# Performance work log

Measured on AMD Instinct MI355X. Metric: run time of the kernel, lower is better.

## Reference

```python
import jax, jax.numpy as jnp
import numpy as np

UNITS = 1024
B, T = 32, 2048


def setup_inputs() -> dict:
    key = jax.random.key(0)
    ks = jax.random.split(key, 8)
    s = 1.0 / np.sqrt(UNITS)
    return {
        "x": jax.random.normal(ks[0], (B, T, UNITS), dtype=jnp.float32),
        "hidden": jax.random.normal(ks[1], (B, UNITS), dtype=jnp.float32),
        "W1_w": jax.random.uniform(ks[2], (UNITS, UNITS), jnp.float32, -s, s),
        "W1_b": jax.random.uniform(ks[3], (UNITS,), jnp.float32, -s, s),
        "W2_w": jax.random.uniform(ks[4], (UNITS, UNITS), jnp.float32, -s, s),
        "W2_b": jax.random.uniform(ks[5], (UNITS,), jnp.float32, -s, s),
        "V_w": jax.random.uniform(ks[6], (1, UNITS), jnp.float32, -s, s),
        "V_b": jax.random.uniform(ks[7], (1,), jnp.float32, -s, s),
    }


def reference(x, hidden, W1_w, W1_b, W2_w, W2_b, V_w, V_b):
    # hidden.squeeze().unsqueeze(1): [B, U] -> [B, 1, U]
    h = hidden[:, None, :]
    # tanh(W1(x) + W2(hidden)): [B, T, U]
    att = jnp.tanh(
        jnp.einsum("btu,vu->btv", x, W1_w) + W1_b
        + jnp.einsum("bsu,vu->bsv", h, W2_w) + W2_b
    )
    # score = V(att): [B, T, 1]
    score = jnp.einsum("btu,ou->bto", att, V_w) + V_b
    # softmax over T, then squeeze().unsqueeze(1): [B, T, 1] -> [B, 1, T]
    attention_weights = jnp.swapaxes(jax.nn.softmax(score, axis=1), 1, 2)
    # bmm([B,1,T], [B,T,U]) -> [B,1,U]; squeeze().unsqueeze(0) -> [1, B, U]
    context_vector = jnp.matmul(attention_weights, x)[:, 0, :][None, :, :]
    return context_vector, attention_weights
```

## Files before the change

kernel.cpp:

```cpp
#include <hip/hip_runtime.h>
#include <hip/hip_bf16.h>
#include <cstdint>
#include <cstddef>

#define UNITS 1024
#define BDIM 32
#define TDIM 2048
#define M_TOT (BDIM*TDIM)
#define KDIM UNITS
#define NDIM UNITS
#define NPART 4

#define K2LOG2E 2.885390081777927f

typedef __attribute__((ext_vector_type(8))) short bf16x8;
typedef __attribute__((ext_vector_type(8))) unsigned short ushort8;
typedef __attribute__((ext_vector_type(4))) float f32x4;

__device__ __forceinline__ unsigned short f2bf(float f) {
  unsigned u = __float_as_uint(f);
  u += 0x7fffu + ((u >> 16) & 1u);
  return (unsigned short)(u >> 16);
}
__device__ __forceinline__ float bf2f(unsigned short h) {
  return __uint_as_float(((unsigned)h) << 16);
}

__global__ __launch_bounds__(256) void cvt_kernel(const float* __restrict__ src,
                                                  ushort* __restrict__ dst, int n8) {
  int i = blockIdx.x * blockDim.x + threadIdx.x;
  int stride = gridDim.x * blockDim.x;
  const float4* s4 = (const float4*)src;
  ushort8* d8 = (ushort8*)dst;
  for (; i < n8; i += stride) {
    float4 a = s4[2*i], b = s4[2*i+1];
    ushort8 o;
    o[0] = f2bf(a.x); o[1] = f2bf(a.y); o[2] = f2bf(a.z); o[3] = f2bf(a.w);
    o[4] = f2bf(b.x); o[5] = f2bf(b.y); o[6] = f2bf(b.z); o[7] = f2bf(b.w);
    d8[i] = o;
  }
}

__global__ __launch_bounds__(64) void prep_c_kernel(const float* __restrict__ W2w,
                                                    const float* __restrict__ hidden,
                                                    const float* __restrict__ W1b,
                                                    const float* __restrict__ W2b,
                                                    float* __restrict__ c) {
  int v = blockIdx.x;
  int l = threadIdx.x;
  float acc[BDIM];
  #pragma unroll
  for (int b = 0; b < BDIM; b++) acc[b] = 0.f;
  for (int u0 = 0; u0 < UNITS; u0 += 64) {
    float w = W2w[v*UNITS + u0 + l];
    #pragma unroll
    for (int b = 0; b < BDIM; b++) acc[b] += w * hidden[b*UNITS + u0 + l];
  }
  float bias = W1b[v] + W2b[v];
  #pragma unroll
  for (int b = 0; b < BDIM; b++) {
    float s = acc[b];
    #pragma unroll
    for (int off = 32; off > 0; off >>= 1) s += __shfl_xor(s, off);
    if (l == 0) c[b*UNITS + v] = s + bias;
  }
}

#define GLL(g, l) __builtin_amdgcn_global_load_lds(                              \
    (const __attribute__((address_space(1))) void*)(g),                          \
    (__attribute__((address_space(3))) void*)(l), 16, 0, 0)

__global__ __launch_bounds__(512, 2) void gemm_score_kernel(
    const ushort* __restrict__ A,
    const ushort* __restrict__ W,
    const float* __restrict__ c,
    const float* __restrict__ Vw,
    float* __restrict__ score)
{
  __shared__ ushort shb[65536];

  const int nt = blockIdx.x & 3;
  const int m0 = (blockIdx.x >> 2) * 256;
  const int n0 = nt * 256;
  const int bb = m0 >> 11;
  const int tid = threadIdx.x;
  const int wave = tid >> 6;
  const int l = tid & 63;
  const int lrow = l & 15;
  const int lq = l >> 4;
  const int wm = (wave >> 2) * 128;
  const int wn = (wave & 3) * 64;

  const int s_g = ((tid & 3) - (tid >> 3)) & 3;
  const ushort* sA = A + (size_t)(m0 + (tid >> 2)) * KDIM + s_g * 8;
  const ushort* sB = W + (size_t)(n0 + (tid >> 2)) * KDIM + s_g * 8;

  const int prot = (lq + (lrow >> 1)) & 3;
  const int a_off = (wm + lrow) * 32 + prot * 8;
  const int b_off = (wn + lrow) * 32 + prot * 8;

  f32x4 acc[8][4];
  #pragma unroll
  for (int i = 0; i < 8; i++)
    #pragma unroll
    for (int j = 0; j < 4; j++) acc[i][j] = (f32x4)0.f;

  #define STAGE_A(TAU, C) {                                                     \
    const ushort* g_ = sA + (TAU) * 64 + (C) * 32;                              \
    ushort* d_ = shb + ((2*(TAU)+(C)) & 3) * 8192 + wave * 512;                 \
    GLL(g_, d_);                                                                \
    GLL(g_ + (size_t)128 * KDIM, d_ + 4096); }
  #define STAGE_B(TAU, C) {                                                     \
    const ushort* g_ = sB + (TAU) * 64 + (C) * 32;                              \
    ushort* d_ = shb + 32768 + ((2*(TAU)+(C)) & 3) * 8192 + wave * 512;         \
    GLL(g_, d_);                                                                \
    GLL(g_ + (size_t)128 * KDIM, d_ + 4096); }

  bf16x8 bv[4];

  #define PHASE(TAU, C, IH, VM, DO_ST, ST_TAU, ST_C) {                          \
    const int aslot_ = ((2*(TAU)+(C)) & 3) * 8192;                              \
    const int bslot_ = 32768 + aslot_;                                          \
    bf16x8 av[4];                                                               \
    if ((IH) == 0) {                                                            \
      _Pragma("unroll")                                                         \
      for (int j = 0; j < 4; j++)                                               \
        bv[j] = *(const bf16x8*)(shb + bslot_ + b_off + j * 512);               \
    }                                                                           \
    _Pragma("unroll")                                                           \
    for (int i = 0; i < 4; i++)                                                 \
      av[i] = *(const bf16x8*)(shb + aslot_ + a_off + ((IH)*4 + i) * 512);      \
    if ((DO_ST) == 1) STAGE_A(ST_TAU, ST_C);                                    \
    if ((DO_ST) == 2) STAGE_B(ST_TAU, ST_C);                                    \
    __builtin_amdgcn_s_barrier();                                               \
    __builtin_amdgcn_s_setprio(1);                                              \
    _Pragma("unroll")                                                           \
    for (int i = 0; i < 4; i++)                                                 \
      _Pragma("unroll")                                                         \
      for (int j = 0; j < 4; j++)                                               \
        acc[(IH)*4 + i][j] =                                                    \
          __builtin_amdgcn_mfma_f32_16x16x32_bf16(av[i], bv[j],                 \
                                                  acc[(IH)*4 + i][j], 0, 0, 0); \
    __builtin_amdgcn_s_setprio(0);                                              \
    if ((VM) == 8) asm volatile("s_waitcnt vmcnt(8)" ::: "memory");             \
    if ((VM) == 4) asm volatile("s_waitcnt vmcnt(4)" ::: "memory");             \
    if ((VM) == 0) asm volatile("s_waitcnt vmcnt(0)" ::: "memory");             \
    __builtin_amdgcn_s_barrier();                                               \
    __builtin_amdgcn_sched_barrier(0);                                          \
  }

  STAGE_A(0, 0); STAGE_B(0, 0);
  STAGE_A(0, 1); STAGE_B(0, 1);
  STAGE_A(1, 0); STAGE_B(1, 0);
  asm volatile("s_waitcnt vmcnt(8)" ::: "memory");
  __builtin_amdgcn_s_barrier();
  __builtin_amdgcn_sched_barrier(0);

  #pragma unroll 1
  for (int tau = 0; tau < 14; ++tau) {
    PHASE(tau, 0, 0, -1, 1, tau + 1, 1);
    PHASE(tau, 0, 1,  8, 2, tau + 1, 1);
    PHASE(tau, 1, 0, -1, 1, tau + 2, 0);
    PHASE(tau, 1, 1,  8, 2, tau + 2, 0);
  }
  PHASE(14, 0, 0, -1, 1, 15, 1);
  PHASE(14, 0, 1,  8, 2, 15, 1);
  PHASE(14, 1, 0, -1, 0, 0, 0);
  PHASE(14, 1, 1,  4, 0, 0, 0);
  PHASE(15, 0, 0, -1, 0, 0, 0);
  PHASE(15, 0, 1,  0, 0, 0, 0);
  PHASE(15, 1, 0, -1, 0, 0, 0);
  PHASE(15, 1, 1, -1, 0, 0, 0);

  #undef PHASE
  #undef STAGE_A
  #undef STAGE_B

  float vw4[4], ck4[4];
  float vws = 0.f;
  #pragma unroll
  for (int j = 0; j < 4; j++) {
    int n = n0 + wn + j * 16 + lrow;
    float v = Vw[n];
    vw4[j] = v;
    vws += v;
    ck4[j] = c[bb * NDIM + n] * K2LOG2E;
  }
  float sacc[8][4];
  #pragma unroll
  for (int i = 0; i < 8; i++)
    #pragma unroll
    for (int r = 0; r < 4; r++) sacc[i][r] = 0.f;
  #pragma unroll
  for (int i = 0; i < 8; i++)
    #pragma unroll
    for (int j = 0; j < 4; j++)
      #pragma unroll
      for (int r = 0; r < 4; r++) {
        float t = __builtin_fmaf(acc[i][j][r], K2LOG2E, ck4[j]);
        float e = __builtin_amdgcn_exp2f(t);
        float rr = __builtin_amdgcn_rcpf(e + 1.f);
        sacc[i][r] = __builtin_fmaf(vw4[j], rr, sacc[i][r]);
      }

  float* sred = (float*)shb;
  #pragma unroll
  for (int i = 0; i < 8; i++)
    #pragma unroll
    for (int r = 0; r < 4; r++) {
      float s = vws - 2.f * sacc[i][r];
      s += __shfl_xor(s, 1);
      s += __shfl_xor(s, 2);
      s += __shfl_xor(s, 4);
      s += __shfl_xor(s, 8);
      if (lrow == 0) sred[wave * 128 + i * 16 + lq * 4 + r] = s;
    }
  __syncthreads();
  if (tid < 256) {
    int mh = tid >> 7;
    int ml = tid & 127;
    float v = sred[mh * 512 + ml] + sred[mh * 512 + 128 + ml]
            + sred[mh * 512 + 256 + ml] + sred[mh * 512 + 384 + ml];
    score[(size_t)nt * M_TOT + m0 + tid] = v;
  }
}

__global__ __launch_bounds__(256) void softmax_kernel(float* __restrict__ sc,
                                                      float* __restrict__ wout) {
  const int b = blockIdx.x;
  const int tid = threadIdx.x;
  float4* s4 = (float4*)(sc + (size_t)b * TDIM);
  float4 v0 = s4[2*tid], v1 = s4[2*tid+1];
  #pragma unroll
  for (int k = 1; k < NPART; k++) {
    const float4* p4 = (const float4*)(sc + (size_t)k * M_TOT + (size_t)b * TDIM);
    float4 u0 = p4[2*tid], u1 = p4[2*tid+1];
    v0.x += u0.x; v0.y += u0.y; v0.z += u0.z; v0.w += u0.w;
    v1.x += u1.x; v1.y += u1.y; v1.z += u1.z; v1.w += u1.w;
  }
  float mx = fmaxf(fmaxf(fmaxf(v0.x,v0.y),fmaxf(v0.z,v0.w)),
                   fmaxf(fmaxf(v1.x,v1.y),fmaxf(v1.z,v1.w)));
  #pragma unroll
  for (int off = 32; off > 0; off >>= 1) mx = fmaxf(mx, __shfl_xor(mx, off));
  __shared__ float redm[4];
  __shared__ float reds[4];
  if ((tid & 63) == 0) redm[tid >> 6] = mx;
  __syncthreads();
  mx = fmaxf(fmaxf(redm[0], redm[1]), fmaxf(redm[2], redm[3]));
  v0.x = __expf(v0.x - mx); v0.y = __expf(v0.y - mx);
  v0.z = __expf(v0.z - mx); v0.w = __expf(v0.w - mx);
  v1.x = __expf(v1.x - mx); v1.y = __expf(v1.y - mx);
  v1.z = __expf(v1.z - mx); v1.w = __expf(v1.w - mx);
  float sum = v0.x+v0.y+v0.z+v0.w+v1.x+v1.y+v1.z+v1.w;
  #pragma unroll
  for (int off = 32; off > 0; off >>= 1) sum += __shfl_xor(sum, off);
  if ((tid & 63) == 0) reds[tid >> 6] = sum;
  __syncthreads();
  sum = reds[0]+reds[1]+reds[2]+reds[3];
  float inv = 1.f / sum;
  v0.x *= inv; v0.y *= inv; v0.z *= inv; v0.w *= inv;
  v1.x *= inv; v1.y *= inv; v1.z *= inv; v1.w *= inv;
  s4[2*tid] = v0; s4[2*tid+1] = v1;
  float4* w4 = (float4*)(wout + (size_t)b * TDIM);
  w4[2*tid] = v0; w4[2*tid+1] = v1;
}

__global__ __launch_bounds__(256) void context_kernel(const ushort* __restrict__ xb,
                                                      const float* __restrict__ wgt,
                                                      float* __restrict__ ctx) {
  const int uc = blockIdx.x;
  const int b = blockIdx.y;
  const int tid = threadIdx.x;
  __shared__ float wl[TDIM];
  {
    const float4* wsrc = (const float4*)(wgt + (size_t)b * TDIM);
    float4* wdst = (float4*)wl;
    wdst[tid] = wsrc[tid];
    wdst[tid + 256] = wsrc[tid + 256];
  }
  __syncthreads();
  const int ut = tid & 15;
  const int tr = tid >> 4;
  const ushort* xp = xb + (size_t)b * TDIM * UNITS + uc * 128 + ut * 8;
  float a8[8];
  #pragma unroll
  for (int e = 0; e < 8; e++) a8[e] = 0.f;
  for (int t = tr; t < TDIM; t += 64) {
    ushort8 x0 = *(const ushort8*)(xp + (size_t)(t     ) * UNITS);
    ushort8 x1 = *(const ushort8*)(xp + (size_t)(t + 16) * UNITS);
    ushort8 x2 = *(const ushort8*)(xp + (size_t)(t + 32) * UNITS);
    ushort8 x3 = *(const ushort8*)(xp + (size_t)(t + 48) * UNITS);
    float w0 = wl[t], w1 = wl[t+16], w2 = wl[t+32], w3 = wl[t+48];
    #pragma unroll
    for (int e = 0; e < 8; e++) {
      a8[e] += w0 * bf2f(x0[e]);
      a8[e] += w1 * bf2f(x1[e]);
      a8[e] += w2 * bf2f(x2[e]);
      a8[e] += w3 * bf2f(x3[e]);
    }
  }
  #pragma unroll
  for (int e = 0; e < 8; e++) {
    a8[e] += __shfl_xor(a8[e], 16);
    a8[e] += __shfl_xor(a8[e], 32);
  }
  __shared__ float red[512];
  const int wave = tid >> 6;
  const int l = tid & 63;
  if (l < 16) {
    #pragma unroll
    for (int e = 0; e < 8; e++) red[wave * 128 + l * 8 + e] = a8[e];
  }
  __syncthreads();
  if (tid < 128) {
    float v = red[tid] + red[128 + tid] + red[256 + tid] + red[384 + tid];
    ctx[(size_t)b * UNITS + uc * 128 + tid] = v;
  }
}

extern "C" void kernel_launch(void* const* d_in, const int* in_sizes, int n_in,
                              void* d_out, int out_size, void* d_ws, size_t ws_size,
                              hipStream_t stream) {
  const float* x   = (const float*)d_in[0];
  const float* hid = (const float*)d_in[1];
  const float* W1w = (const float*)d_in[2];
  const float* W1b = (const float*)d_in[3];
  const float* W2w = (const float*)d_in[4];
  const float* W2b = (const float*)d_in[5];
  const float* Vw  = (const float*)d_in[6];
  float* out = (float*)d_out;

  char* ws = (char*)d_ws;
  ushort* xb   = (ushort*)ws;
  ushort* w1b  = (ushort*)(ws + (size_t)M_TOT*KDIM*2);
  float*  cbuf = (float*)(ws + (size_t)M_TOT*KDIM*2 + (size_t)NDIM*KDIM*2);
  float*  score= (float*)((char*)cbuf + (size_t)BDIM*NDIM*4);

  cvt_kernel<<<4096, 256, 0, stream>>>(x, xb, M_TOT*KDIM/8);
  cvt_kernel<<<512, 256, 0, stream>>>(W1w, w1b, NDIM*KDIM/8);
  prep_c_kernel<<<NDIM, 64, 0, stream>>>(W2w, hid, W1b, W2b, cbuf);
  gemm_score_kernel<<<M_TOT/256 * NPART, 512, 0, stream>>>(xb, w1b, cbuf, Vw, score);
  softmax_kernel<<<BDIM, 256, 0, stream>>>(score, out + (size_t)BDIM*UNITS);
  context_kernel<<<dim3(8, BDIM), 256, 0, stream>>>(xb, score, out);
}
```

Before: 562.8 us.

## Shrink GEMM tile to 128x256 with 3-stage K=32 pipeline for higher occupancy

```diff
diff --git a/kernel.cpp b/kernel.cpp
--- a/kernel.cpp
+++ b/kernel.cpp
@@ -70,17 +70,17 @@
     (const __attribute__((address_space(1))) void*)(g),                          \
     (__attribute__((address_space(3))) void*)(l), 16, 0, 0)
 
-__global__ __launch_bounds__(512, 2) void gemm_score_kernel(
+__global__ __launch_bounds__(512, 4) void gemm_score_kernel(
     const ushort* __restrict__ A,
     const ushort* __restrict__ W,
     const float* __restrict__ c,
     const float* __restrict__ Vw,
     float* __restrict__ score)
 {
-  __shared__ ushort shb[65536];
+  __shared__ ushort shb[36864];
 
   const int nt = blockIdx.x & 3;
-  const int m0 = (blockIdx.x >> 2) * 256;
+  const int m0 = (blockIdx.x >> 2) * 128;
   const int n0 = nt * 256;
   const int bb = m0 >> 11;
   const int tid = threadIdx.x;
@@ -88,93 +88,70 @@
   const int l = tid & 63;
   const int lrow = l & 15;
   const int lq = l >> 4;
-  const int wm = (wave >> 2) * 128;
+  const int wm = (wave >> 2) * 64;
   const int wn = (wave & 3) * 64;
 
   const int s_g = ((tid & 3) - (tid >> 3)) & 3;
-  const ushort* sA = A + (size_t)(m0 + (tid >> 2)) * KDIM + s_g * 8;
-  const ushort* sB = W + (size_t)(n0 + (tid >> 2)) * KDIM + s_g * 8;
+  const ushort* gA = A + (size_t)(m0 + (tid >> 2)) * KDIM + s_g * 8;
+  const ushort* gB = W + (size_t)(n0 + (tid >> 2)) * KDIM + s_g * 8;
 
   const int prot = (lq + (lrow >> 1)) & 3;
   const int a_off = (wm + lrow) * 32 + prot * 8;
-  const int b_off = (wn + lrow) * 32 + prot * 8;
-
-  f32x4 acc[8][4];
-  #pragma unroll
-  for (int i = 0; i < 8; i++)
+  const int b_off = 12288 + (wn >> 7) * 4096 + ((wn & 64) + lrow) * 32 + prot * 8;
+
+  f32x4 acc[4][4];
+  #pragma unroll
+  for (int i = 0; i < 4; i++)
     #pragma unroll
     for (int j = 0; j < 4; j++) acc[i][j] = (f32x4)0.f;
 
-  #define STAGE_A(TAU, C) {                                                     \
-    const ushort* g_ = sA + (TAU) * 64 + (C) * 32;                              \
-    ushort* d_ = shb + ((2*(TAU)+(C)) & 3) * 8192 + wave * 512;                 \
-    GLL(g_, d_);                                                                \
-    GLL(g_ + (size_t)128 * KDIM, d_ + 4096); }
-  #define STAGE_B(TAU, C) {                                                     \
-    const ushort* g_ = sB + (TAU) * 64 + (C) * 32;                              \
-    ushort* d_ = shb + 32768 + ((2*(TAU)+(C)) & 3) * 8192 + wave * 512;         \
-    GLL(g_, d_);                                                                \
-    GLL(g_ + (size_t)128 * KDIM, d_ + 4096); }
-
-  bf16x8 bv[4];
-
-  #define PHASE(TAU, C, IH, VM, DO_ST, ST_TAU, ST_C) {                          \
-    const int aslot_ = ((2*(TAU)+(C)) & 3) * 8192;                              \
-    const int bslot_ = 32768 + aslot_;                                          \
-    bf16x8 av[4];                                                               \
-    if ((IH) == 0) {                                                            \
-      _Pragma("unroll")                                                         \
-      for (int j = 0; j < 4; j++)                                               \
-        bv[j] = *(const bf16x8*)(shb + bslot_ + b_off + j * 512);               \
-    }                                                                           \
+  #define STAGE(SL) {                                                           \
+    GLL(gA, shb + (SL) * 4096 + wave * 512);                                    \
+    GLL(gB, shb + 12288 + (SL) * 8192 + wave * 512);                            \
+    GLL(gB + (size_t)128 * KDIM, shb + 12288 + (SL) * 8192 + 4096 + wave * 512);\
+    gA += 32; gB += 32; }
+
+  #define PHASE(SR, SW, VM, DO_ST) {                                           \
+    bf16x8 av[4], bv[4];                                                        \
     _Pragma("unroll")                                                           \
     for (int i = 0; i < 4; i++)                                                 \
-      av[i] = *(const bf16x8*)(shb + aslot_ + a_off + ((IH)*4 + i) * 512);      \
-    if ((DO_ST) == 1) STAGE_A(ST_TAU, ST_C);                                    \
-    if ((DO_ST) == 2) STAGE_B(ST_TAU, ST_C);                                    \
+      av[i] = *(const bf16x8*)(shb + (SR) * 4096 + a_off + i * 512);            \
+    _Pragma("unroll")                                                           \
+    for (int j = 0; j < 4; j++)                                                 \
+      bv[j] = *(const bf16x8*)(shb + (SR) * 8192 + b_off + j * 512);            \
+    if (DO_ST) STAGE(SW);                                                       \
     __builtin_amdgcn_s_barrier();                                               \
     __builtin_amdgcn_s_setprio(1);                                              \
     _Pragma("unroll")                                                           \
     for (int i = 0; i < 4; i++)                                                 \
       _Pragma("unroll")                                                         \
       for (int j = 0; j < 4; j++)                                               \
-        acc[(IH)*4 + i][j] =                                                    \
-          __builtin_amdgcn_mfma_f32_16x16x32_bf16(av[i], bv[j],                 \
-                                                  acc[(IH)*4 + i][j], 0, 0, 0); \
+        acc[i][j] = __builtin_amdgcn_mfma_f32_16x16x32_bf16(av[i], bv[j],       \
+                                                            acc[i][j], 0, 0, 0);\
     __builtin_amdgcn_s_setprio(0);                                              \
-    if ((VM) == 8) asm volatile("s_waitcnt vmcnt(8)" ::: "memory");             \
-    if ((VM) == 4) asm volatile("s_waitcnt vmcnt(4)" ::: "memory");             \
+    if ((VM) == 3) asm volatile("s_waitcnt vmcnt(3)" ::: "memory");             \
     if ((VM) == 0) asm volatile("s_waitcnt vmcnt(0)" ::: "memory");             \
     __builtin_amdgcn_s_barrier();                                               \
     __builtin_amdgcn_sched_barrier(0);                                          \
   }
 
-  STAGE_A(0, 0); STAGE_B(0, 0);
-  STAGE_A(0, 1); STAGE_B(0, 1);
-  STAGE_A(1, 0); STAGE_B(1, 0);
-  asm volatile("s_waitcnt vmcnt(8)" ::: "memory");
+  STAGE(0);
+  STAGE(1);
+  asm volatile("s_waitcnt vmcnt(3)" ::: "memory");
   __builtin_amdgcn_s_barrier();
   __builtin_amdgcn_sched_barrier(0);
 
   #pragma unroll 1
-  for (int tau = 0; tau < 14; ++tau) {
-    PHASE(tau, 0, 0, -1, 1, tau + 1, 1);
-    PHASE(tau, 0, 1,  8, 2, tau + 1, 1);
-    PHASE(tau, 1, 0, -1, 1, tau + 2, 0);
-    PHASE(tau, 1, 1,  8, 2, tau + 2, 0);
-  }
-  PHASE(14, 0, 0, -1, 1, 15, 1);
-  PHASE(14, 0, 1,  8, 2, 15, 1);
-  PHASE(14, 1, 0, -1, 0, 0, 0);
-  PHASE(14, 1, 1,  4, 0, 0, 0);
-  PHASE(15, 0, 0, -1, 0, 0, 0);
-  PHASE(15, 0, 1,  0, 0, 0, 0);
-  PHASE(15, 1, 0, -1, 0, 0, 0);
-  PHASE(15, 1, 1, -1, 0, 0, 0);
+  for (int t = 0; t < 10; ++t) {
+    PHASE(0, 2, 3, 1);
+    PHASE(1, 0, 3, 1);
+    PHASE(2, 1, 3, 1);
+  }
+  PHASE(0, 0, 0, 0);
+  PHASE(1, 0, -1, 0);
 
   #undef PHASE
-  #undef STAGE_A
-  #undef STAGE_B
+  #undef STAGE
 
   float vw4[4], ck4[4];
   float vws = 0.f;
@@ -186,13 +163,13 @@
     vws += v;
     ck4[j] = c[bb * NDIM + n] * K2LOG2E;
   }
-  float sacc[8][4];
-  #pragma unroll
-  for (int i = 0; i < 8; i++)
+  float sacc[4][4];
+  #pragma unroll
+  for (int i = 0; i < 4; i++)
     #pragma unroll
     for (int r = 0; r < 4; r++) sacc[i][r] = 0.f;
   #pragma unroll
-  for (int i = 0; i < 8; i++)
+  for (int i = 0; i < 4; i++)
     #pragma unroll
     for (int j = 0; j < 4; j++)
       #pragma unroll
@@ -205,7 +182,7 @@
 
   float* sred = (float*)shb;
   #pragma unroll
-  for (int i = 0; i < 8; i++)
+  for (int i = 0; i < 4; i++)
     #pragma unroll
     for (int r = 0; r < 4; r++) {
       float s = vws - 2.f * sacc[i][r];
@@ -213,14 +190,14 @@
       s += __shfl_xor(s, 2);
       s += __shfl_xor(s, 4);
       s += __shfl_xor(s, 8);
-      if (lrow == 0) sred[wave * 128 + i * 16 + lq * 4 + r] = s;
+      if (lrow == 0) sred[wave * 64 + i * 16 + lq * 4 + r] = s;
     }
   __syncthreads();
-  if (tid < 256) {
-    int mh = tid >> 7;
-    int ml = tid & 127;
-    float v = sred[mh * 512 + ml] + sred[mh * 512 + 128 + ml]
-            + sred[mh * 512 + 256 + ml] + sred[mh * 512 + 384 + ml];
+  if (tid < 128) {
+    int mh = tid >> 6;
+    int ml = tid & 63;
+    float v = sred[(mh * 4 + 0) * 64 + ml] + sred[(mh * 4 + 1) * 64 + ml]
+            + sred[(mh * 4 + 2) * 64 + ml] + sred[(mh * 4 + 3) * 64 + ml];
     score[(size_t)nt * M_TOT + m0 + tid] = v;
   }
 }
@@ -339,7 +316,7 @@
   cvt_kernel<<<4096, 256, 0, stream>>>(x, xb, M_TOT*KDIM/8);
   cvt_kernel<<<512, 256, 0, stream>>>(W1w, w1b, NDIM*KDIM/8);
   prep_c_kernel<<<NDIM, 64, 0, stream>>>(W2w, hid, W1b, W2b, cbuf);
-  gemm_score_kernel<<<M_TOT/256 * NPART, 512, 0, stream>>>(xb, w1b, cbuf, Vw, score);
+  gemm_score_kernel<<<M_TOT/128 * NPART, 512, 0, stream>>>(xb, w1b, cbuf, Vw, score);
   softmax_kernel<<<BDIM, 256, 0, stream>>>(score, out + (size_t)BDIM*UNITS);
   context_kernel<<<dim3(8, BDIM), 256, 0, stream>>>(xb, score, out);
 }
```

New measurement: 565.9 us. No clear change (+0.6%).

## Software-pipeline LDS fragment reads across phases with double-buffered B registers

Applied to the files above, without the earlier changes.

```diff
diff --git a/kernel.cpp b/kernel.cpp
--- a/kernel.cpp
+++ b/kernel.cpp
@@ -105,76 +105,106 @@
     #pragma unroll
     for (int j = 0; j < 4; j++) acc[i][j] = (f32x4)0.f;
 
-  #define STAGE_A(TAU, C) {                                                     \
-    const ushort* g_ = sA + (TAU) * 64 + (C) * 32;                              \
-    ushort* d_ = shb + ((2*(TAU)+(C)) & 3) * 8192 + wave * 512;                 \
-    GLL(g_, d_);                                                                \
-    GLL(g_ + (size_t)128 * KDIM, d_ + 4096); }
-  #define STAGE_B(TAU, C) {                                                     \
-    const ushort* g_ = sB + (TAU) * 64 + (C) * 32;                              \
-    ushort* d_ = shb + 32768 + ((2*(TAU)+(C)) & 3) * 8192 + wave * 512;         \
-    GLL(g_, d_);                                                                \
-    GLL(g_ + (size_t)128 * KDIM, d_ + 4096); }
-
-  bf16x8 bv[4];
-
-  #define PHASE(TAU, C, IH, VM, DO_ST, ST_TAU, ST_C) {                          \
-    const int aslot_ = ((2*(TAU)+(C)) & 3) * 8192;                              \
-    const int bslot_ = 32768 + aslot_;                                          \
-    bf16x8 av[4];                                                               \
-    if ((IH) == 0) {                                                            \
-      _Pragma("unroll")                                                         \
-      for (int j = 0; j < 4; j++)                                               \
-        bv[j] = *(const bf16x8*)(shb + bslot_ + b_off + j * 512);               \
-    }                                                                           \
-    _Pragma("unroll")                                                           \
-    for (int i = 0; i < 4; i++)                                                 \
-      av[i] = *(const bf16x8*)(shb + aslot_ + a_off + ((IH)*4 + i) * 512);      \
-    if ((DO_ST) == 1) STAGE_A(ST_TAU, ST_C);                                    \
-    if ((DO_ST) == 2) STAGE_B(ST_TAU, ST_C);                                    \
+  bf16x8 avlo[4], avhi[4], bv0[4], bv1[4];
+
+  #define RDA(SL, I) (*(const bf16x8*)(shb + (SL) * 8192 + a_off + (I) * 512))
+  #define RDB(SL, J) (*(const bf16x8*)(shb + 32768 + (SL) * 8192 + b_off + (J) * 512))
+
+  #define STA(SL, KO) { const ushort* g_ = sA + (KO);                           \
+    GLL(g_, shb + (SL) * 8192 + wave * 512);                                    \
+    GLL(g_ + (size_t)128 * KDIM, shb + (SL) * 8192 + 4096 + wave * 512); }
+  #define STB(SL, KO) { const ushort* g_ = sB + (KO);                           \
+    GLL(g_, shb + 32768 + (SL) * 8192 + wave * 512);                            \
+    GLL(g_ + (size_t)128 * KDIM, shb + 32768 + (SL) * 8192 + 4096 + wave * 512); }
+  #define STN ((void)0)
+
+  #define VMW(VM) {                                                             \
+    if ((VM) == 6) asm volatile("s_waitcnt vmcnt(6)" ::: "memory");             \
+    if ((VM) == 4) asm volatile("s_waitcnt vmcnt(4)" ::: "memory");             \
+    if ((VM) == 0) asm volatile("s_waitcnt vmcnt(0)" ::: "memory"); }
+
+  #define PH1(RS, BV, STx, VM) {                                                \
+    avhi[0] = RDA(RS, 4); avhi[1] = RDA(RS, 5);                                 \
+    avhi[2] = RDA(RS, 6); avhi[3] = RDA(RS, 7);                                 \
+    STx;                                                                        \
+    __builtin_amdgcn_sched_barrier(0);                                          \
     __builtin_amdgcn_s_barrier();                                               \
+    asm volatile("s_waitcnt lgkmcnt(4)" ::: "memory");                          \
     __builtin_amdgcn_s_setprio(1);                                              \
     _Pragma("unroll")                                                           \
     for (int i = 0; i < 4; i++)                                                 \
       _Pragma("unroll")                                                         \
       for (int j = 0; j < 4; j++)                                               \
-        acc[(IH)*4 + i][j] =                                                    \
-          __builtin_amdgcn_mfma_f32_16x16x32_bf16(av[i], bv[j],                 \
-                                                  acc[(IH)*4 + i][j], 0, 0, 0); \
+        acc[i][j] = __builtin_amdgcn_mfma_f32_16x16x32_bf16(avlo[i], BV[j],     \
+                                                            acc[i][j], 0, 0, 0);\
     __builtin_amdgcn_s_setprio(0);                                              \
-    if ((VM) == 8) asm volatile("s_waitcnt vmcnt(8)" ::: "memory");             \
-    if ((VM) == 4) asm volatile("s_waitcnt vmcnt(4)" ::: "memory");             \
-    if ((VM) == 0) asm volatile("s_waitcnt vmcnt(0)" ::: "memory");             \
+    VMW(VM);                                                                    \
     __builtin_amdgcn_s_barrier();                                               \
+    __builtin_amdgcn_sched_barrier(0); }
+
+  #define PH2(RSA, RSB, BNEW, BCUR, STx, VM, DO_RD) {                           \
+    if (DO_RD) {                                                                \
+      BNEW[0] = RDB(RSB, 0); BNEW[1] = RDB(RSB, 1);                             \
+      BNEW[2] = RDB(RSB, 2); BNEW[3] = RDB(RSB, 3);                             \
+      avlo[0] = RDA(RSA, 0); avlo[1] = RDA(RSA, 1);                             \
+      avlo[2] = RDA(RSA, 2); avlo[3] = RDA(RSA, 3);                             \
+    }                                                                           \
+    STx;                                                                        \
     __builtin_amdgcn_sched_barrier(0);                                          \
-  }
-
-  STAGE_A(0, 0); STAGE_B(0, 0);
-  STAGE_A(0, 1); STAGE_B(0, 1);
-  STAGE_A(1, 0); STAGE_B(1, 0);
+    __builtin_amdgcn_s_barrier();                                               \
+    if (DO_RD) { asm volatile("s_waitcnt lgkmcnt(8)" ::: "memory"); }           \
+    else       { asm volatile("s_waitcnt lgkmcnt(0)" ::: "memory"); }           \
+    __builtin_amdgcn_s_setprio(1);                                              \
+    _Pragma("unroll")                                                           \
+    for (int i = 0; i < 4; i++)                                                 \
+      _Pragma("unroll")                                                         \
+      for (int j = 0; j < 4; j++)                                               \
+        acc[4 + i][j] = __builtin_amdgcn_mfma_f32_16x16x32_bf16(avhi[i],        \
+                                         BCUR[j], acc[4 + i][j], 0, 0, 0);      \
+    __builtin_amdgcn_s_setprio(0);                                              \
+    VMW(VM);                                                                    \
+    __builtin_amdgcn_s_barrier();                                               \
+    __builtin_amdgcn_sched_barrier(0); }
+
+  STA(0, 0);  STB(0, 0);
+  STA(1, 32); STB(1, 32);
+  STA(2, 64); STB(2, 64);
   asm volatile("s_waitcnt vmcnt(8)" ::: "memory");
   __builtin_amdgcn_s_barrier();
   __builtin_amdgcn_sched_barrier(0);
+  bv0[0] = RDB(0, 0); bv0[1] = RDB(0, 1); bv0[2] = RDB(0, 2); bv0[3] = RDB(0, 3);
+  avlo[0] = RDA(0, 0); avlo[1] = RDA(0, 1); avlo[2] = RDA(0, 2); avlo[3] = RDA(0, 3);
+  __builtin_amdgcn_sched_barrier(0);
 
   #pragma unroll 1
-  for (int tau = 0; tau < 14; ++tau) {
-    PHASE(tau, 0, 0, -1, 1, tau + 1, 1);
-    PHASE(tau, 0, 1,  8, 2, tau + 1, 1);
-    PHASE(tau, 1, 0, -1, 1, tau + 2, 0);
-    PHASE(tau, 1, 1,  8, 2, tau + 2, 0);
-  }
-  PHASE(14, 0, 0, -1, 1, 15, 1);
-  PHASE(14, 0, 1,  8, 2, 15, 1);
-  PHASE(14, 1, 0, -1, 0, 0, 0);
-  PHASE(14, 1, 1,  4, 0, 0, 0);
-  PHASE(15, 0, 0, -1, 0, 0, 0);
-  PHASE(15, 0, 1,  0, 0, 0, 0);
-  PHASE(15, 1, 0, -1, 0, 0, 0);
-  PHASE(15, 1, 1, -1, 0, 0, 0);
-
-  #undef PHASE
-  #undef STAGE_A
-  #undef STAGE_B
+  for (int t = 0; t < 7; ++t) {
+    PH1(0, bv0, STA(3, 96),  6);
+    PH2(1, 1, bv1, bv0, STB(3, 96), -1, 1);
+    PH1(1, bv1, STA(0, 128), 6);
+    PH2(2, 2, bv0, bv1, STB(0, 128), -1, 1);
+    PH1(2, bv0, STA(1, 160), 6);
+    PH2(3, 3, bv1, bv0, STB(1, 160), -1, 1);
+    PH1(3, bv1, STA(2, 192), 6);
+    PH2(0, 0, bv0, bv1, STB(2, 192), -1, 1);
+    sA += 128; sB += 128;
+  }
+  PH1(0, bv0, STA(3, 96), 6);
+  PH2(1, 1, bv1, bv0, STB(3, 96), -1, 1);
+  PH1(1, bv1, STN, 4);
+  PH2(2, 2, bv0, bv1, STN, -1, 1);
+  PH1(2, bv0, STN, 0);
+  PH2(3, 3, bv1, bv0, STN, -1, 1);
+  PH1(3, bv1, STN, -1);
+  PH2(0, 0, bv0, bv1, STN, -1, 0);
+
+  #undef PH1
+  #undef PH2
+  #undef STA
+  #undef STB
+  #undef STN
+  #undef VMW
+  #undef RDA
+  #undef RDB
 
   float vw4[4], ck4[4];
   float vws = 0.f;
```

Result: no change. 564.2 us (+0.3%).
